# Kernel tuning notes

Measured on AMD Instinct MI355X. Metric: run time of the kernel, lower is better.

## Reference

```python
import jax, jax.numpy as jnp
import numpy as np

EPS_PEN = 1e-05


def _penalty(x):
    return jnp.sqrt(x + EPS_PEN)


def _warp(img, flow):
    """Bilinear warp (Resample2d): sample img at (x+u, y+v), clamped borders.
    img: (B,C,H,W), flow: (B,2,H,W) -> (B,C,H,W)."""
    B, C, H, W = img.shape
    xs = jnp.arange(W, dtype=flow.dtype)[None, None, :]  # (1,1,W)
    ys = jnp.arange(H, dtype=flow.dtype)[None, :, None]  # (1,H,1)
    x = xs + flow[:, 0]  # (B,H,W)
    y = ys + flow[:, 1]
    x0f = jnp.floor(x)
    y0f = jnp.floor(y)
    wx = x - x0f  # bilinear weights
    wy = y - y0f
    x0 = jnp.clip(x0f.astype(jnp.int32), 0, W - 1)
    x1 = jnp.clip(x0 + 1, 0, W - 1)
    y0 = jnp.clip(y0f.astype(jnp.int32), 0, H - 1)
    y1 = jnp.clip(y0 + 1, 0, H - 1)
    img_flat = img.reshape(B, C, H * W)

    def gather(yi, xi):
        idx = (yi * W + xi).reshape(B, 1, H * W)
        idx = jnp.broadcast_to(idx, (B, C, H * W))
        return jnp.take_along_axis(img_flat, idx, axis=2).reshape(B, C, H, W)

    v00 = gather(y0, x0)
    v01 = gather(y0, x1)
    v10 = gather(y1, x0)
    v11 = gather(y1, x1)
    wx = wx[:, None]  # (B,1,H,W)
    wy = wy[:, None]
    return ((1 - wy) * ((1 - wx) * v00 + wx * v01)
            + wy * ((1 - wx) * v10 + wx * v11))


def _energy(flow, img1, img2, alpha=1.0, beta=1.0):
    img2_warp = _warp(img2, flow)
    A = jnp.sum((img1 - img2_warp) ** 2, axis=1)          # (B,H,W)
    data_term = jnp.sum(_penalty(A), axis=(1, 2))          # (B,)
    # conv with kernel_dx == horizontal forward diff per channel; dy vertical
    dx = flow[:, :, :, 1:] - flow[:, :, :, :-1]            # (B,2,H,W-1)
    dy = flow[:, :, 1:, :] - flow[:, :, :-1, :]            # (B,2,H-1,W)
    Bx = jnp.pad(jnp.sum(dx ** 2, axis=1), ((0, 0), (0, 0), (0, 1)))
    By = jnp.pad(jnp.sum(dy ** 2, axis=1), ((0, 0), (0, 1), (0, 0)))
    smooth_term = jnp.sum(_penalty(Bx + By), axis=(1, 2))  # (B,)
    return alpha * data_term + beta * smooth_term


def setup_inputs() -> dict:
    key = jax.random.key(0)
    ks = jax.random.split(key, 6)
    B, H, W = 16, 448, 1024
    mean = jax.random.normal(ks[0], (B, 2, H, W), dtype=jnp.float32)
    log_var = jax.random.normal(ks[1], (B, 2, H, W), dtype=jnp.float32)
    img1 = jax.random.uniform(ks[2], (B, 3, H, W), dtype=jnp.float32)
    img2 = jax.random.uniform(ks[3], (B, 3, H, W), dtype=jnp.float32)
    target = jax.random.normal(ks[4], (B, 2, H, W), dtype=jnp.float32)
    eps = jax.random.normal(ks[5], (B, 2, H, W), dtype=jnp.float32)
    return {"mean": mean, "log_var": log_var, "img1": img1, "img2": img2,
            "target": target, "eps": eps}


def reference(mean, log_var, img1, img2, target, eps):
    # reparam: z = mean + exp(log_var/2) * eps  (eps replaces Normal(0,1).sample)
    flow_sample = mean + jnp.exp(log_var / 2.0) * eps
    elbo = _energy(flow_sample, img1, img2) - jnp.sum(log_var, axis=(1, 2, 3)) / 2.0
    mean_elbo = jnp.mean(elbo)
    # elementwise EPE: L2 norm over flow channels of (mean - target)
    epe = jnp.sqrt(jnp.sum((mean - target) ** 2, axis=1))
    mean_epe = jnp.mean(epe)
    return (mean_elbo, mean_epe)
```

## Files before the change

kernel.cpp:

```cpp
#include <hip/hip_runtime.h>

#define BB 16
#define HH 448
#define WW 1024
constexpr int HW    = HH * WW;
constexpr int TOTAL = BB * HW;
constexpr int NBLK  = 7168;
constexpr int NTHR  = 256;

__device__ __forceinline__ float flow_at(const float* __restrict__ mean,
                                         const float* __restrict__ lv,
                                         const float* __restrict__ eps,
                                         int idx) {
    return mean[idx] + __expf(0.5f * lv[idx]) * eps[idx];
}

__global__ __launch_bounds__(NTHR) void elbo_main(
    const float* __restrict__ mean, const float* __restrict__ lv,
    const float* __restrict__ img1, const float* __restrict__ img2,
    const float* __restrict__ target, const float* __restrict__ eps,
    float2* __restrict__ partials)
{
    const int tid  = blockIdx.x * blockDim.x + threadIdx.x;
    const int nthr = gridDim.x * blockDim.x;

    float se = 0.0f;
    float sp = 0.0f;

    for (int p = tid; p < TOTAL; p += nthr) {
        const int b = p / HW;
        const int r = p - b * HW;
        const int y = r >> 10;
        const int x = r & (WW - 1);

        const int base = b * 2 * HW + r;

        const float m0 = mean[base],       m1 = mean[base + HW];
        const float l0 = lv[base],         l1 = lv[base + HW];
        const float e0 = eps[base],        e1 = eps[base + HW];
        const float u = m0 + __expf(0.5f * l0) * e0;
        const float v = m1 + __expf(0.5f * l1) * e1;

        float dx2 = 0.0f, dy2 = 0.0f;
        if (x < WW - 1) {
            const float ur = flow_at(mean, lv, eps, base + 1);
            const float vr = flow_at(mean, lv, eps, base + HW + 1);
            const float a = ur - u, c = vr - v;
            dx2 = a * a + c * c;
        }
        if (y < HH - 1) {
            const float ud = flow_at(mean, lv, eps, base + WW);
            const float vd = flow_at(mean, lv, eps, base + HW + WW);
            const float a = ud - u, c = vd - v;
            dy2 = a * a + c * c;
        }
        const float smooth = sqrtf(dx2 + dy2 + 1e-5f);

        const float xs = (float)x + u;
        const float ys = (float)y + v;
        const float x0f = floorf(xs), y0f = floorf(ys);
        const float wx = xs - x0f,    wy = ys - y0f;
        int x0 = (int)x0f; x0 = min(max(x0, 0), WW - 1);
        const int x1 = min(x0 + 1, WW - 1);
        int y0 = (int)y0f; y0 = min(max(y0, 0), HH - 1);
        const int y1 = min(y0 + 1, HH - 1);

        const int b3  = b * 3 * HW;
        const int i00 = y0 * WW + x0, i01 = y0 * WW + x1;
        const int i10 = y1 * WW + x0, i11 = y1 * WW + x1;

        float A = 0.0f;
        #pragma unroll
        for (int c = 0; c < 3; ++c) {
            const int o = b3 + c * HW;
            const float v00 = img2[o + i00];
            const float v01 = img2[o + i01];
            const float v10 = img2[o + i10];
            const float v11 = img2[o + i11];
            const float top = v00 + wx * (v01 - v00);
            const float bot = v10 + wx * (v11 - v10);
            const float w   = top + wy * (bot - top);
            const float d   = img1[o + r] - w;
            A += d * d;
        }
        const float data = sqrtf(A + 1e-5f);

        const float t0 = target[base], t1 = target[base + HW];
        const float du = m0 - t0, dv = m1 - t1;
        const float epe = sqrtf(du * du + dv * dv);

        se += data + smooth - 0.5f * (l0 + l1);
        sp += epe;
    }

    #pragma unroll
    for (int off = 32; off > 0; off >>= 1) {
        se += __shfl_down(se, off);
        sp += __shfl_down(sp, off);
    }
    __shared__ float s_e[NTHR / 64], s_p[NTHR / 64];
    const int lane = threadIdx.x & 63;
    const int wid  = threadIdx.x >> 6;
    if (lane == 0) { s_e[wid] = se; s_p[wid] = sp; }
    __syncthreads();
    if (threadIdx.x == 0) {
        float te = 0.0f, tp = 0.0f;
        #pragma unroll
        for (int i = 0; i < NTHR / 64; ++i) { te += s_e[i]; tp += s_p[i]; }
        partials[blockIdx.x] = make_float2(te, tp);
    }
}

__global__ __launch_bounds__(256) void elbo_final(
    const float2* __restrict__ partials, float* __restrict__ out)
{
    double se = 0.0, sp = 0.0;
    for (int i = threadIdx.x; i < NBLK; i += 256) {
        const float2 v = partials[i];
        se += (double)v.x;
        sp += (double)v.y;
    }
    #pragma unroll
    for (int off = 32; off > 0; off >>= 1) {
        se += __shfl_down(se, off);
        sp += __shfl_down(sp, off);
    }
    __shared__ double s_e[4], s_p[4];
    const int lane = threadIdx.x & 63;
    const int wid  = threadIdx.x >> 6;
    if (lane == 0) { s_e[wid] = se; s_p[wid] = sp; }
    __syncthreads();
    if (threadIdx.x == 0) {
        double te = 0.0, tp = 0.0;
        #pragma unroll
        for (int i = 0; i < 4; ++i) { te += s_e[i]; tp += s_p[i]; }
        out[0] = (float)(te / (double)BB);
        out[1] = (float)(tp / (double)TOTAL);
    }
}

extern "C" void kernel_launch(void* const* d_in, const int* in_sizes, int n_in,
                              void* d_out, int out_size, void* d_ws, size_t ws_size,
                              hipStream_t stream) {
    const float* mean   = (const float*)d_in[0];
    const float* logvar = (const float*)d_in[1];
    const float* img1   = (const float*)d_in[2];
    const float* img2   = (const float*)d_in[3];
    const float* target = (const float*)d_in[4];
    const float* eps    = (const float*)d_in[5];
    float* out = (float*)d_out;
    float2* partials = (float2*)d_ws;

    elbo_main<<<NBLK, NTHR, 0, stream>>>(mean, logvar, img1, img2, target, eps, partials);
    elbo_final<<<1, 256, 0, stream>>>(partials, out);
}
```

Measured before the change: 403.0 us.

## Tile elbo kernel by row groups with float4 loads and rolling flow reuse

```diff
diff --git a/kernel.cpp b/kernel.cpp
--- a/kernel.cpp
+++ b/kernel.cpp
@@ -4,93 +4,153 @@
 #define HH 448
 #define WW 1024
 constexpr int HW    = HH * WW;
-constexpr int TOTAL = BB * HW;
-constexpr int NBLK  = 7168;
+constexpr int ROWS  = 4;
+constexpr int RGRP  = HH / ROWS;
+constexpr int NBLK  = BB * RGRP;
 constexpr int NTHR  = 256;
-
-__device__ __forceinline__ float flow_at(const float* __restrict__ mean,
-                                         const float* __restrict__ lv,
-                                         const float* __restrict__ eps,
-                                         int idx) {
-    return mean[idx] + __expf(0.5f * lv[idx]) * eps[idx];
-}
+constexpr long long TOTAL = (long long)BB * HW;
+
 
 __global__ __launch_bounds__(NTHR) void elbo_main(
-    const float* __restrict__ mean, const float* __restrict__ lv,
+    const float* __restrict__ mean, const float* __restrict__ lvar,
     const float* __restrict__ img1, const float* __restrict__ img2,
     const float* __restrict__ target, const float* __restrict__ eps,
     float2* __restrict__ partials)
 {
-    const int tid  = blockIdx.x * blockDim.x + threadIdx.x;
-    const int nthr = gridDim.x * blockDim.x;
-
-    float se = 0.0f;
-    float sp = 0.0f;
-
-    for (int p = tid; p < TOTAL; p += nthr) {
-        const int b = p / HW;
-        const int r = p - b * HW;
-        const int y = r >> 10;
-        const int x = r & (WW - 1);
-
-        const int base = b * 2 * HW + r;
-
-        const float m0 = mean[base],       m1 = mean[base + HW];
-        const float l0 = lv[base],         l1 = lv[base + HW];
-        const float e0 = eps[base],        e1 = eps[base + HW];
-        const float u = m0 + __expf(0.5f * l0) * e0;
-        const float v = m1 + __expf(0.5f * l1) * e1;
-
-        float dx2 = 0.0f, dy2 = 0.0f;
-        if (x < WW - 1) {
-            const float ur = flow_at(mean, lv, eps, base + 1);
-            const float vr = flow_at(mean, lv, eps, base + HW + 1);
-            const float a = ur - u, c = vr - v;
-            dx2 = a * a + c * c;
-        }
-        if (y < HH - 1) {
-            const float ud = flow_at(mean, lv, eps, base + WW);
-            const float vd = flow_at(mean, lv, eps, base + HW + WW);
-            const float a = ud - u, c = vd - v;
-            dy2 = a * a + c * c;
-        }
-        const float smooth = sqrtf(dx2 + dy2 + 1e-5f);
-
-        const float xs = (float)x + u;
-        const float ys = (float)y + v;
-        const float x0f = floorf(xs), y0f = floorf(ys);
-        const float wx = xs - x0f,    wy = ys - y0f;
-        int x0 = (int)x0f; x0 = min(max(x0, 0), WW - 1);
-        const int x1 = min(x0 + 1, WW - 1);
-        int y0 = (int)y0f; y0 = min(max(y0, 0), HH - 1);
-        const int y1 = min(y0 + 1, HH - 1);
-
-        const int b3  = b * 3 * HW;
-        const int i00 = y0 * WW + x0, i01 = y0 * WW + x1;
-        const int i10 = y1 * WW + x0, i11 = y1 * WW + x1;
-
-        float A = 0.0f;
+    constexpr int NXCD = 8, CPX = NBLK / NXCD;
+    const int wg = (blockIdx.x % NXCD) * CPX + blockIdx.x / NXCD;
+
+    const int b  = wg / RGRP;
+    const int y0 = (wg - b * RGRP) * ROWS;
+    const int t  = threadIdx.x;
+    const int x  = t << 2;
+
+    const int fbase = b * 2 * HW;
+    const int ibase = b * 3 * HW;
+
+    float se = 0.f;
+    float sp = 0.f;
+
+    float u[4], v[4], un[4], vn[4];
+
+    auto load_flow = [&](int y, float* uu, float* vv, bool contrib) {
+        const int o = fbase + y * WW + x;
+        const float4 m0 = *(const float4*)(mean + o);
+        const float4 m1 = *(const float4*)(mean + o + HW);
+        const float4 l0 = *(const float4*)(lvar + o);
+        const float4 l1 = *(const float4*)(lvar + o + HW);
+        const float4 e0 = *(const float4*)(eps  + o);
+        const float4 e1 = *(const float4*)(eps  + o + HW);
+        uu[0] = m0.x + __expf(0.5f * l0.x) * e0.x;
+        uu[1] = m0.y + __expf(0.5f * l0.y) * e0.y;
+        uu[2] = m0.z + __expf(0.5f * l0.z) * e0.z;
+        uu[3] = m0.w + __expf(0.5f * l0.w) * e0.w;
+        vv[0] = m1.x + __expf(0.5f * l1.x) * e1.x;
+        vv[1] = m1.y + __expf(0.5f * l1.y) * e1.y;
+        vv[2] = m1.z + __expf(0.5f * l1.z) * e1.z;
+        vv[3] = m1.w + __expf(0.5f * l1.w) * e1.w;
+        if (contrib) {
+            const float4 t0 = *(const float4*)(target + o);
+            const float4 t1 = *(const float4*)(target + o + HW);
+            float du, dv;
+            du = m0.x - t0.x; dv = m1.x - t1.x; sp += sqrtf(du*du + dv*dv);
+            du = m0.y - t0.y; dv = m1.y - t1.y; sp += sqrtf(du*du + dv*dv);
+            du = m0.z - t0.z; dv = m1.z - t1.z; sp += sqrtf(du*du + dv*dv);
+            du = m0.w - t0.w; dv = m1.w - t1.w; sp += sqrtf(du*du + dv*dv);
+            se -= 0.5f * (l0.x + l0.y + l0.z + l0.w +
+                          l1.x + l1.y + l1.z + l1.w);
+        }
+    };
+
+    load_flow(y0, u, v, true);
+
+    for (int r = 0; r < ROWS; ++r) {
+        const int y = y0 + r;
+        const bool have_dn = (y + 1) < HH;
+        if (have_dn) load_flow(y + 1, un, vn, r < ROWS - 1);
+
+        float uR = __shfl_down(u[0], 1);
+        float vR = __shfl_down(v[0], 1);
+        if (((t & 63) == 63) && (t != NTHR - 1)) {
+            const int o = fbase + y * WW + x + 4;
+            uR = mean[o]      + __expf(0.5f * lvar[o])      * eps[o];
+            vR = mean[o + HW] + __expf(0.5f * lvar[o + HW]) * eps[o + HW];
+        }
+
+        const int ro = y * WW + x;
+        const float4 g0 = *(const float4*)(img1 + ibase + ro);
+        const float4 g1 = *(const float4*)(img1 + ibase + HW + ro);
+        const float4 g2 = *(const float4*)(img1 + ibase + 2 * HW + ro);
+        const float i1c0[4] = {g0.x, g0.y, g0.z, g0.w};
+        const float i1c1[4] = {g1.x, g1.y, g1.z, g1.w};
+        const float i1c2[4] = {g2.x, g2.y, g2.z, g2.w};
+
+        const float* __restrict__ p2 = img2 + ibase;
+
         #pragma unroll
-        for (int c = 0; c < 3; ++c) {
-            const int o = b3 + c * HW;
-            const float v00 = img2[o + i00];
-            const float v01 = img2[o + i01];
-            const float v10 = img2[o + i10];
-            const float v11 = img2[o + i11];
-            const float top = v00 + wx * (v01 - v00);
-            const float bot = v10 + wx * (v11 - v10);
-            const float w   = top + wy * (bot - top);
-            const float d   = img1[o + r] - w;
-            A += d * d;
-        }
-        const float data = sqrtf(A + 1e-5f);
-
-        const float t0 = target[base], t1 = target[base + HW];
-        const float du = m0 - t0, dv = m1 - t1;
-        const float epe = sqrtf(du * du + dv * dv);
-
-        se += data + smooth - 0.5f * (l0 + l1);
-        sp += epe;
+        for (int i = 0; i < 4; ++i) {
+            const float ui = u[i], vi = v[i];
+            const int gx = x + i;
+
+            float dx2 = 0.f, dy2 = 0.f;
+            if (gx < WW - 1) {
+                const float ur = (i < 3) ? u[i + 1] : uR;
+                const float vr = (i < 3) ? v[i + 1] : vR;
+                const float a = ur - ui, c = vr - vi;
+                dx2 = a * a + c * c;
+            }
+            if (have_dn) {
+                const float a = un[i] - ui, c = vn[i] - vi;
+                dy2 = a * a + c * c;
+            }
+            se += sqrtf(dx2 + dy2 + 1e-5f);
+
+            const float xs = (float)gx + ui;
+            const float ys = (float)y  + vi;
+            const float x0f = floorf(xs), y0f = floorf(ys);
+            const float wx = xs - x0f,    wy = ys - y0f;
+            int x0 = (int)x0f; x0 = min(max(x0, 0), WW - 1);
+            const int x1 = min(x0 + 1, WW - 1);
+            int yy0 = (int)y0f; yy0 = min(max(yy0, 0), HH - 1);
+            const int yy1 = min(yy0 + 1, HH - 1);
+            const int i00 = yy0 * WW + x0, i01 = yy0 * WW + x1;
+            const int i10 = yy1 * WW + x0, i11 = yy1 * WW + x1;
+
+            float A = 0.f;
+            {
+                const float v00 = p2[i00], v01 = p2[i01];
+                const float v10 = p2[i10], v11 = p2[i11];
+                const float top = v00 + wx * (v01 - v00);
+                const float bot = v10 + wx * (v11 - v10);
+                const float w   = top + wy * (bot - top);
+                const float d   = i1c0[i] - w;
+                A += d * d;
+            }
+            {
+                const float v00 = p2[HW + i00], v01 = p2[HW + i01];
+                const float v10 = p2[HW + i10], v11 = p2[HW + i11];
+                const float top = v00 + wx * (v01 - v00);
+                const float bot = v10 + wx * (v11 - v10);
+                const float w   = top + wy * (bot - top);
+                const float d   = i1c1[i] - w;
+                A += d * d;
+            }
+            {
+                const float v00 = p2[2*HW + i00], v01 = p2[2*HW + i01];
+                const float v10 = p2[2*HW + i10], v11 = p2[2*HW + i11];
+                const float top = v00 + wx * (v01 - v00);
+                const float bot = v10 + wx * (v11 - v10);
+                const float w   = top + wy * (bot - top);
+                const float d   = i1c2[i] - w;
+                A += d * d;
+            }
+            se += sqrtf(A + 1e-5f);
+        }
+
+        if (r < ROWS - 1) {
+            #pragma unroll
+            for (int i = 0; i < 4; ++i) { u[i] = un[i]; v[i] = vn[i]; }
+        }
     }
 
     #pragma unroll
```

After: 470.9 us. 16.9% more time.
